# Kernel optimization log

Measured on AMD Instinct MI355X. Metric: run time of the kernel, lower is better.

## Reference

```python
import jax, jax.numpy as jnp
import numpy as np
from jax import lax

B, CH, TS = 64, 9, 3000
D, H, EMB = 64, 256, 32
WIDTHS = (3, 2, 2, 2, 2, 2)
IN_CH = (1, H, H, H, H, H)
OUT_CH = (H, H, H, H, H, D)


def setup_inputs():
    keys = iter(jax.random.split(jax.random.key(0), 64))
    inp = {"x": jax.random.normal(next(keys), (B, CH, TS), jnp.float32)}
    for l, (ci, co, w) in enumerate(zip(IN_CH, OUT_CH, WIDTHS)):
        inp[f"conv_w{l}"] = jax.random.normal(next(keys), (co, ci, w), jnp.float32) / np.float32(np.sqrt(ci * w))
        inp[f"conv_b{l}"] = jnp.zeros((co,), jnp.float32)
        inp[f"gn_g{l}"] = jnp.ones((co,), jnp.float32)
        inp[f"gn_b{l}"] = jnp.zeros((co,), jnp.float32)
    inp["ro_w"] = jax.random.normal(next(keys), (D, D), jnp.float32) / np.float32(np.sqrt(D))
    inp["ro_b"] = jnp.zeros((D,), jnp.float32)
    for r in range(2):
        inp[f"msg_w{r}"] = jax.random.normal(next(keys), (2 * D, D), jnp.float32) / np.float32(np.sqrt(2 * D))
        inp[f"msg_b{r}"] = jnp.zeros((D,), jnp.float32)
    inp["rn_w1"] = jax.random.normal(next(keys), (D, D), jnp.float32) / np.float32(np.sqrt(D))
    inp["rn_b1"] = jnp.zeros((D,), jnp.float32)
    inp["rn_w2"] = jax.random.normal(next(keys), (D, D), jnp.float32) / np.float32(np.sqrt(D))
    inp["rn_b2"] = jnp.zeros((D,), jnp.float32)
    inp["proj_w"] = jax.random.normal(next(keys), (D, EMB), jnp.float32) / np.float32(np.sqrt(D))
    inp["proj_b"] = jnp.zeros((EMB,), jnp.float32)
    return inp


def _gn(h, g, b):
    # GroupNorm(num_groups=1): normalize over (C, T) per sample
    mu = h.mean(axis=(1, 2), keepdims=True)
    var = h.var(axis=(1, 2), keepdims=True)
    return (h - mu) * lax.rsqrt(var + 1e-5) * g[None, :, None] + b[None, :, None]


def _forward(x, ps):
    b, ch, ts = x.shape
    h = x.reshape(b * ch, 1, ts)  # each view is one 1-channel node signal
    for l, w in enumerate(WIDTHS):
        W, bi, g, be = ps[4 * l], ps[4 * l + 1], ps[4 * l + 2], ps[4 * l + 3]
        h = lax.conv_general_dilated(h, W, (w,), [(w // 2, w // 2)], dimension_numbers=("NCH", "OIH", "NCH")) + bi[None, :, None]
        h = jax.nn.gelu(_gn(h, g, be), approximate=False)
    ro_w, ro_b = ps[24], ps[25]
    h = jnp.einsum("nct,co->not", h, ro_w) + ro_b[None, :, None]  # 1x1 readout conv
    lat = h.transpose(0, 2, 1)  # [b*ch, T, D]
    N = b * ch
    # fully-connected graph within each sample, exactly as in the torch code
    msg_from = np.repeat(np.arange(N), ch - 1)
    grid = np.broadcast_to(np.arange(N).reshape(b, ch)[:, None, :], (b, ch, ch))
    msg_to = grid[:, ~np.eye(ch, dtype=bool)].reshape(-1)
    for W, bi in ((ps[26], ps[27]), (ps[28], ps[29])):
        m = jnp.concatenate([lat[msg_from], lat[msg_to]], axis=-1)  # [E, T, 2D]
        m = jax.nn.relu(m @ W + bi) / (ch - 1)  # dropout is identity at eval
        lat = lat.at[msg_to].add(m)
    view_id = np.repeat(np.arange(b), ch)
    y = jax.ops.segment_sum(lat, view_id, num_segments=b)  # [b, T, D]
    y = (jax.nn.relu(y @ ps[30] + ps[31]) @ ps[32] + ps[33]) / ch
    return (y @ ps[34] + ps[35]).transpose(0, 2, 1)  # [b, EMB, T]


def reference(x, conv_w0, conv_b0, gn_g0, gn_b0, conv_w1, conv_b1, gn_g1, gn_b1, conv_w2, conv_b2, gn_g2, gn_b2, conv_w3, conv_b3, gn_g3, gn_b3, conv_w4, conv_b4, gn_g4, gn_b4, conv_w5, conv_b5, gn_g5, gn_b5, ro_w, ro_b, msg_w0, msg_b0, msg_w1, msg_b1, rn_w1, rn_b1, rn_w2, rn_b2, proj_w, proj_b):
    ps = (conv_w0, conv_b0, gn_g0, gn_b0, conv_w1, conv_b1, gn_g1, gn_b1, conv_w2, conv_b2, gn_g2, gn_b2, conv_w3, conv_b3, gn_g3, gn_b3, conv_w4, conv_b4, gn_g4, gn_b4, conv_w5, conv_b5, gn_g5, gn_b5, ro_w, ro_b, msg_w0, msg_b0, msg_w1, msg_b1, rn_w1, rn_b1, rn_w2, rn_b2, proj_w, proj_b)
    return _forward(x, ps)
```

## Files before the change

### kernel.cpp

```cpp
#include <hip/hip_runtime.h>
#include <hip/hip_bf16.h>

typedef __hip_bfloat16 bf16;
typedef __attribute__((ext_vector_type(8))) short s8v;
typedef __attribute__((ext_vector_type(4))) float f4v;

__device__ __forceinline__ float erf_approx(float x) {
    float ax = fabsf(x);
    float t = __builtin_amdgcn_rcpf(__builtin_fmaf(0.3275911f, ax, 1.0f));
    float p = t * (0.254829592f + t * (-0.284496736f + t * (1.421413741f
              + t * (-1.453152027f + t * 1.061405429f))));
    float r = 1.0f - p * __expf(-ax * ax);
    return copysignf(r, x);
}
__device__ __forceinline__ float gelu_f(float v) {
    return 0.5f * v * (1.f + erf_approx(v * 0.70710678118654752440f));
}
__device__ __forceinline__ unsigned short f2bf_u(float f) {
    bf16 b = __float2bfloat16(f);
    return *(unsigned short*)&b;
}
__device__ __forceinline__ float bfu2f(unsigned short u) {
    bf16 b = *(bf16*)&u;
    return __bfloat162float(b);
}

__global__ __launch_bounds__(256) void zero_k(float* __restrict__ p, int n) {
    int i = blockIdx.x * 256 + threadIdx.x;
    if (i < n) p[i] = 0.f;
}

__global__ __launch_bounds__(256) void wcvt_k(
    const float* __restrict__ w1, const float* __restrict__ w2,
    const float* __restrict__ w3, const float* __restrict__ w4,
    const float* __restrict__ w5, bf16* __restrict__ dst)
{
    int i = blockIdx.x * 256 + threadIdx.x;
    if (i >= 557056) return;
    const float* src; int li;
    if      (i < 131072) { src = w1; li = i; }
    else if (i < 262144) { src = w2; li = i - 131072; }
    else if (i < 393216) { src = w3; li = i - 262144; }
    else if (i < 524288) { src = w4; li = i - 393216; }
    else                 { src = w5; li = i - 524288; }
    int co = li >> 9, rem = li & 511;
    int kc = rem >> 6, rr = rem & 63;
    int s = rr >> 5, cil = rr & 31;
    dst[i] = __float2bfloat16(src[co * 512 + (kc * 32 + cil) * 2 + s]);
}

__global__ __launch_bounds__(256) void m0red_k(
    const float* __restrict__ W0, const float* __restrict__ b0, float* __restrict__ coef)
{
    __shared__ float red[256];
    const int co = threadIdx.x;
    float w0 = W0[3 * co], w1 = W0[3 * co + 1], w2 = W0[3 * co + 2], b = b0[co];
    float vals[14] = {w0, w1, w2, b,
                      w0 * w0, w1 * w1, w2 * w2, b * b,
                      2.f * w0 * w1, 2.f * w0 * w2, 2.f * w1 * w2,
                      2.f * w0 * b, 2.f * w1 * b, 2.f * w2 * b};
    for (int k = 0; k < 14; k++) {
        red[co] = vals[k];
        __syncthreads();
        for (int st = 128; st > 0; st >>= 1) {
            if (co < st) red[co] += red[co + st];
            __syncthreads();
        }
        if (co == 0) coef[k] = red[0];
        __syncthreads();
    }
}

__global__ __launch_bounds__(256) void c0stats_k(
    const float* __restrict__ x, const float* __restrict__ coef,
    float* __restrict__ mu0, float* __restrict__ rstd0)
{
    __shared__ float xsl[3008];
    __shared__ float red[512];
    const int n = blockIdx.x, tid = threadIdx.x;
    const float* xr = x + (size_t)n * 3000;
    for (int i = tid; i < 750; i += 256) *(float4*)&xsl[4 + 4 * i] = *(const float4*)(xr + 4 * i);
    if (tid < 4) xsl[tid] = 0.f;
    float c[14];
    #pragma unroll
    for (int k = 0; k < 14; k++) c[k] = coef[k];
    __syncthreads();
    float S = 0.f, Q = 0.f;
    if (tid < 250) {
        float f[16];
        #pragma unroll
        for (int k = 0; k < 4; k++) *(float4*)&f[4 * k] = *(const float4*)&xsl[12 * tid + 4 * k];
        #pragma unroll
        for (int j = 0; j < 4; j++) {
            float x0 = f[3 * j + 3], x1 = f[3 * j + 4], x2 = f[3 * j + 5];
            S += c[0] * x0 + c[1] * x1 + c[2] * x2 + c[3];
            Q += c[4] * x0 * x0 + c[5] * x1 * x1 + c[6] * x2 * x2 + c[7]
               + c[8] * x0 * x1 + c[9] * x0 * x2 + c[10] * x1 * x2
               + c[11] * x0 + c[12] * x1 + c[13] * x2;
        }
    }
    red[tid] = S; red[256 + tid] = Q;
    __syncthreads();
    for (int st = 128; st > 0; st >>= 1) {
        if (tid < st) { red[tid] += red[tid + st]; red[256 + tid] += red[256 + tid + st]; }
        __syncthreads();
    }
    if (tid == 0) {
        float m = red[0] * (1.f / 256000.f);
        float var = red[256] * (1.f / 256000.f) - m * m;
        mu0[n] = m;
        rstd0[n] = rsqrtf(var + 1e-5f);
    }
}

__global__ __launch_bounds__(256) void h0gT_k(
    const float* __restrict__ x, const float* __restrict__ W0,
    const float* __restrict__ b0, const float* __restrict__ g0,
    const float* __restrict__ be0, const float* __restrict__ mu0,
    const float* __restrict__ rstd0, bf16* __restrict__ h0gT, int n0)
{
    __shared__ float xs[96];
    __shared__ float w0s[768];
    __shared__ float aco[256], cco[256];
    const int z = blockIdx.y;
    const int n = n0 + z;
    const int t0 = blockIdx.x * 32;
    const int tid = threadIdx.x;
    for (int i = tid; i < 768; i += 256) w0s[i] = W0[i];
    {
        float mu = mu0[n], rs = rstd0[n];
        float a = rs * g0[tid];
        aco[tid] = a;
        cco[tid] = (b0[tid] - mu) * a + be0[tid];
    }
    if (tid < 96) {
        int xg = 3 * t0 - 1 + tid;
        xs[tid] = (xg >= 0 && xg < 3000) ? x[(size_t)n * 3000 + xg] : 0.f;
    }
    __syncthreads();
    const int oct = tid & 31, ci0 = oct * 8;
    const int tq = tid >> 5;
    #pragma unroll
    for (int u = 0; u < 4; u++) {
        int tl = tq + 8 * u;
        int t = t0 + tl;
        if (t >= 1000) continue;
        float x0 = xs[3 * tl], x1 = xs[3 * tl + 1], x2 = xs[3 * tl + 2];
        ushort4 lo, hi;
        unsigned short* pu = (unsigned short*)&lo;
        #pragma unroll
        for (int jj = 0; jj < 8; jj++) {
            int ci = ci0 + jj;
            float conv = w0s[3 * ci] * x0 + w0s[3 * ci + 1] * x1 + w0s[3 * ci + 2] * x2;
            float v = gelu_f(conv * aco[ci] + cco[ci]);
            if (jj < 4) pu[jj] = f2bf_u(v);
            else ((unsigned short*)&hi)[jj - 4] = f2bf_u(v);
        }
        bf16* orow = h0gT + ((size_t)z * 1000 + t) * 256 + ci0;
        *(ushort4*)orow = lo;
        *(ushort4*)(orow + 4) = hi;
    }
}

template<int MW, int NW, bool FUSE>
__global__ __launch_bounds__(256) void convT_k(
    const bf16* __restrict__ g, const bf16* __restrict__ Wp,
    const float* __restrict__ bias, bf16* __restrict__ hout,
    float* __restrict__ ssum, float* __restrict__ ssq,
    int T_g, int T_out, int n0,
    const float* __restrict__ pssum, const float* __restrict__ pssq,
    const float* __restrict__ pgam, const float* __restrict__ pbet,
    float pinvCT)
{
    constexpr int CO = 4 * NW * 16;
    constexpr int MT = MW * 16;
    constexpr int NSLOT = MT * 8;
    constexpr int NU = (NSLOT + 255) / 256;
    __shared__ bf16 aT[MT * 64];
    __shared__ float biasS[CO];
    __shared__ float red[512];
    __shared__ float acoS[256], ccoS[256];
    const int n  = blockIdx.y;
    const int t0 = blockIdx.x * MT;
    const int tid = threadIdx.x;
    for (int i = tid; i < CO; i += 256) biasS[i] = bias[i];
    if (FUSE) {
        float mu = pssum[n0 + n] * pinvCT;
        float rs = rsqrtf(pssq[n0 + n] * pinvCT - mu * mu + 1e-5f);
        float a = rs * pgam[tid];
        acoS[tid] = a;
        ccoS[tid] = pbet[tid] - mu * a;
        __syncthreads();
    }
    const int w = tid >> 6, lane = tid & 63;
    const int l16 = lane & 15, quad = lane >> 4;
    const int sx = l16 & 7;
    const bf16* gb = g + (size_t)n * T_g * 256;

    bool s_inv[NU];
    int s_q[NU], s_tin[NU], s_off[NU];
    #pragma unroll
    for (int u = 0; u < NU; u++) {
        int slot = tid + 256 * u;
        s_inv[u] = (NSLOT % 256 != 0) && (slot >= NSLOT);
        if (s_inv[u]) { s_tin[u] = 0x7fffffff; s_q[u] = 0; s_off[u] = 0; continue; }
        int t = slot >> 3, j = slot & 7;
        int ks = j >> 2, q = j & 3;
        s_q[u] = q;
        s_tin[u] = 2 * (t0 + t) - 1 + ks;
        s_off[u] = (t * 8 + (j ^ (t & 7))) * 8;
    }

    f4v acc[MW][NW];
    #pragma unroll
    for (int i = 0; i < MW; i++)
        #pragma unroll
        for (int j = 0; j < NW; j++) acc[i][j] = (f4v){0.f, 0.f, 0.f, 0.f};

    auto act8 = [&](s8v v, int ci0) -> s8v {
        if (FUSE) {
            float4 a0 = *(const float4*)&acoS[ci0], a1 = *(const float4*)&acoS[ci0 + 4];
            float4 c0 = *(const float4*)&ccoS[ci0], c1 = *(const float4*)&ccoS[ci0 + 4];
            float av[8] = {a0.x, a0.y, a0.z, a0.w, a1.x, a1.y, a1.z, a1.w};
            float cv[8] = {c0.x, c0.y, c0.z, c0.w, c1.x, c1.y, c1.z, c1.w};
            unsigned short* uu = (unsigned short*)&v;
            #pragma unroll
            for (int jj = 0; jj < 8; jj++)
                uu[jj] = f2bf_u(gelu_f(bfu2f(uu[jj]) * av[jj] + cv[jj]));
        }
        return v;
    };

    for (int kc = 0; kc < 8; kc++) {
        #pragma unroll
        for (int u = 0; u < NU; u++) {
            if (s_inv[u]) continue;
            int tin = s_tin[u];
            s8v v = (s8v){0, 0, 0, 0, 0, 0, 0, 0};
            if ((unsigned)tin < (unsigned)T_g)
                v = act8(*(const s8v*)(gb + (size_t)tin * 256 + kc * 32 + s_q[u] * 8),
                         kc * 32 + s_q[u] * 8);
            *(s8v*)&aT[s_off[u]] = v;
        }
        s8v bfr[2][NW];
        #pragma unroll
        for (int ks = 0; ks < 2; ks++)
            #pragma unroll
            for (int j = 0; j < NW; j++) {
                int co = w * NW * 16 + j * 16 + l16;
                bfr[ks][j] = *(const s8v*)(Wp + (size_t)co * 512 + kc * 64 + ks * 32 + quad * 8);
            }
        __syncthreads();
        #pragma unroll
        for (int ks = 0; ks < 2; ks++) {
            const int sl = (ks * 4 + quad) ^ sx;
            s8v af[MW];
            #pragma unroll
            for (int i = 0; i < MW; i++)
                af[i] = *(const s8v*)&aT[(i * 16 + l16) * 64 + sl * 8];
            #pragma unroll
            for (int i = 0; i < MW; i++)
                #pragma unroll
                for (int j = 0; j < NW; j++)
                    acc[i][j] = __builtin_amdgcn_mfma_f32_16x16x32_bf16(af[i], bfr[ks][j], acc[i][j], 0, 0, 0);
        }
        __syncthreads();
    }

    float lsum = 0.f, lsq = 0.f;
    #pragma unroll
    for (int i = 0; i < MW; i++) {
        #pragma unroll
        for (int r = 0; r < 4; r++) {
            int t = t0 + i * 16 + quad * 4 + r;
            if (t < T_out) {
                bf16* orow = hout + ((size_t)n * T_out + t) * CO;
                #pragma unroll
                for (int j = 0; j < NW; j++) {
                    int co = w * NW * 16 + j * 16 + l16;
                    float v = acc[i][j][r] + biasS[co];
                    orow[co] = __float2bfloat16(v);
                    lsum += v; lsq += v * v;
                }
            }
        }
    }
    red[tid] = lsum; red[256 + tid] = lsq;
    __syncthreads();
    for (int st = 128; st > 0; st >>= 1) {
        if (tid < st) { red[tid] += red[tid + st]; red[256 + tid] += red[256 + tid + st]; }
        __syncthreads();
    }
    if (tid == 0) { atomicAdd(&ssum[n0 + n], red[0]); atomicAdd(&ssq[n0 + n], red[256]); }
}

__global__ __launch_bounds__(256) void readout_pre_k(
    const bf16* __restrict__ h5T, const float* __restrict__ row,
    const float* __restrict__ rob, const float* __restrict__ g5,
    const float* __restrict__ be5, const float* __restrict__ ssum,
    const float* __restrict__ ssq, float invCT,
    const float* __restrict__ mw, const float* __restrict__ mb,
    float* __restrict__ lat0, float* __restrict__ A0, float* __restrict__ Bv0)
{
    __shared__ float lh[2112];
    __shared__ float ll[2112];
    __shared__ float lw[8192];
    __shared__ float lb[64];
    const int n = blockIdx.x, tid = threadIdx.x;
    const float mu = ssum[n] * invCT;
    const float rs = rsqrtf(ssq[n] * invCT - mu * mu + 1e-5f);
    for (int idx = tid; idx < 2112; idx += 256) {
        int c = idx & 63;
        float a = rs * g5[c];
        float v = __bfloat162float(h5T[(size_t)n * 2112 + idx]) * a + (be5[c] - mu * a);
        lh[idx] = gelu_f(v);
    }
    for (int idx = tid; idx < 4096; idx += 256) lw[idx] = row[idx];
    if (tid < 64) lb[tid] = rob[tid];
    __syncthreads();
    for (int idx = tid; idx < 2112; idx += 256) {
        int t = idx >> 6, d = idx & 63;
        float a = lb[d];
        #pragma unroll 8
        for (int c = 0; c < 64; c++) a += lh[t * 64 + c] * lw[c * 64 + d];
        ll[idx] = a;
        lat0[(size_t)n * 2112 + idx] = a;
    }
    __syncthreads();
    for (int idx = tid; idx < 8192; idx += 256) lw[idx] = mw[idx];
    if (tid < 64) lb[tid] = mb[tid];
    __syncthreads();
    for (int idx = tid; idx < 2112; idx += 256) {
        int t = idx >> 6, d = idx & 63;
        float a = 0.f, bb = lb[d];
        #pragma unroll 8
        for (int k = 0; k < 64; k++) {
            float xv = ll[t * 64 + k];
            a  += xv * lw[k * 64 + d];
            bb += xv * lw[(64 + k) * 64 + d];
        }
        A0[(size_t)n * 2112 + idx]  = a;
        Bv0[(size_t)n * 2112 + idx] = bb;
    }
}

__global__ __launch_bounds__(256) void comb_pre_k(
    const float* __restrict__ lat0, const float* __restrict__ A0,
    const float* __restrict__ Bv0, const float* __restrict__ mw,
    const float* __restrict__ mb, float* __restrict__ lat1,
    float* __restrict__ A1, float* __restrict__ Bv1)
{
    __shared__ float ll[2112];
    __shared__ float lw[8192];
    __shared__ float lb[64];
    const int n = blockIdx.x, tid = threadIdx.x;
    const int b9 = (n / 9) * 9, j = n - b9;
    for (int idx = tid; idx < 2112; idx += 256) {
        float base = Bv0[(size_t)n * 2112 + idx];
        float s = 0.f;
        #pragma unroll
        for (int i = 0; i < 9; i++) {
            if (i == j) continue;
            s += fmaxf(A0[(size_t)(b9 + i) * 2112 + idx] + base, 0.f);
        }
        float v = lat0[(size_t)n * 2112 + idx] + s * 0.125f;
        ll[idx] = v;
        lat1[(size_t)n * 2112 + idx] = v;
    }
    for (int idx = tid; idx < 8192; idx += 256) lw[idx] = mw[idx];
    if (tid < 64) lb[tid] = mb[tid];
    __syncthreads();
    for (int idx = tid; idx < 2112; idx += 256) {
        int t = idx >> 6, d = idx & 63;
        float a = 0.f, bb = lb[d];
        #pragma unroll 8
        for (int k = 0; k < 64; k++) {
            float xv = ll[t * 64 + k];
            a  += xv * lw[k * 64 + d];
            bb += xv * lw[(64 + k) * 64 + d];
        }
        A1[(size_t)n * 2112 + idx]  = a;
        Bv1[(size_t)n * 2112 + idx] = bb;
    }
}

__global__ __launch_bounds__(256) void final2_k(
    const float* __restrict__ lat1, const float* __restrict__ A1,
    const float* __restrict__ Bv1,
    const float* __restrict__ w1, const float* __restrict__ b1,
    const float* __restrict__ w2, const float* __restrict__ b2,
    const float* __restrict__ pw, const float* __restrict__ pb,
    float* __restrict__ out)
{
    __shared__ float ly[2112], lz[2112];
    __shared__ float lw1[4096], lw2[4096], lpw[2048];
    __shared__ float lb1[64], lb2[64], lpb[32];
    const int b = blockIdx.x, tid = threadIdx.x;
    for (int idx = tid; idx < 4096; idx += 256) { lw1[idx] = w1[idx]; lw2[idx] = w2[idx]; }
    for (int idx = tid; idx < 2048; idx += 256) lpw[idx] = pw[idx];
    if (tid < 64) { lb1[tid] = b1[tid]; lb2[tid] = b2[tid]; }
    if (tid < 32) lpb[tid] = pb[tid];
    for (int idx = tid; idx < 2112; idx += 256) {
        float Av[9], Bb[9], s = 0.f;
        #pragma unroll
        for (int jj = 0; jj < 9; jj++) {
            size_t off = ((size_t)(b * 9 + jj)) * 2112 + idx;
            Av[jj] = A1[off];
            Bb[jj] = Bv1[off];
            s += lat1[off];
        }
        float m = 0.f;
        #pragma unroll
        for (int jj = 0; jj < 9; jj++) {
            float rowsum = 0.f;
            #pragma unroll
            for (int ii = 0; ii < 9; ii++) rowsum += fmaxf(Av[ii] + Bb[jj], 0.f);
            m += rowsum - fmaxf(Av[jj] + Bb[jj], 0.f);
        }
        ly[idx] = s + m * 0.125f;
    }
    __syncthreads();
    for (int idx = tid; idx < 2112; idx += 256) {
        int t = idx >> 6, d = idx & 63;
        float s = lb1[d];
        #pragma unroll 8
        for (int k = 0; k < 64; k++) s += ly[t * 64 + k] * lw1[k * 64 + d];
        lz[idx] = fmaxf(s, 0.f);
    }
    __syncthreads();
    for (int idx = tid; idx < 2112; idx += 256) {
        int t = idx >> 6, d = idx & 63;
        float s = lb2[d];
        #pragma unroll 8
        for (int k = 0; k < 64; k++) s += lz[t * 64 + k] * lw2[k * 64 + d];
        ly[idx] = s * (1.f / 9.f);
    }
    __syncthreads();
    for (int idx = tid; idx < 1056; idx += 256) {
        int e = idx / 33, t = idx - e * 33;
        float s = lpb[e];
        #pragma unroll 8
        for (int d = 0; d < 64; d++) s += ly[t * 64 + d] * lpw[d * 32 + e];
        out[(size_t)b * 1056 + idx] = s;
    }
}

extern "C" void kernel_launch(void* const* d_in, const int* in_sizes, int n_in,
                              void* d_out, int out_size, void* d_ws, size_t ws_size,
                              hipStream_t stream)
{
    const float* x = (const float*)d_in[0];
    const float* cw[6]; const float* cb[6]; const float* gg[6]; const float* gb[6];
    for (int l = 0; l < 6; l++) {
        cw[l] = (const float*)d_in[1 + 4 * l];
        cb[l] = (const float*)d_in[2 + 4 * l];
        gg[l] = (const float*)d_in[3 + 4 * l];
        gb[l] = (const float*)d_in[4 + 4 * l];
    }
    const float* ro_w = (const float*)d_in[25];
    const float* ro_b = (const float*)d_in[26];
    const float* mw0  = (const float*)d_in[27];
    const float* mb0  = (const float*)d_in[28];
    const float* mw1  = (const float*)d_in[29];
    const float* mb1  = (const float*)d_in[30];
    const float* rw1  = (const float*)d_in[31];
    const float* rb1  = (const float*)d_in[32];
    const float* rw2  = (const float*)d_in[33];
    const float* rb2  = (const float*)d_in[34];
    const float* pw   = (const float*)d_in[35];
    const float* pb   = (const float*)d_in[36];

    char* ws = (char*)d_ws;
    bf16* h1T  = (bf16*)(ws);
    bf16* h0gT = (bf16*)(ws + 147750912);
    bf16* h2T  = (bf16*)(ws + 147750912);
    bf16* h3T  = (bf16*)(ws + 221773824);
    bf16* h4T  = (bf16*)(ws);
    bf16* h5T  = (bf16*)(ws + 147750912);
    float* lat0 = (float*)(ws);
    float* A0   = lat0 + 1216512;
    float* Bv0  = A0   + 1216512;
    float* lat1 = Bv0  + 1216512;
    float* A1   = lat1 + 1216512;
    float* Bv1  = A1   + 1216512;
    float* stat  = (float*)(ws + 258932736);
    float* mu0   = stat;
    float* rstd0 = stat + 576;
    float* coef  = stat + 1152;
    float* ssumA = stat + 1168;
    float* ssqA  = ssumA + 5 * 576;
    bf16*  Wp    = (bf16*)(ws + 258965504);
    #define SSUM(l) (ssumA + ((l) - 1) * 576)
    #define SSQ(l)  (ssqA  + ((l) - 1) * 576)

    zero_k<<<(5760 + 255) / 256, 256, 0, stream>>>(ssumA, 2 * 5 * 576);
    wcvt_k<<<(557056 + 255) / 256, 256, 0, stream>>>(cw[1], cw[2], cw[3], cw[4], cw[5], Wp);
    m0red_k<<<1, 256, 0, stream>>>(cw[0], cb[0], coef);
    c0stats_k<<<576, 256, 0, stream>>>(x, coef, mu0, rstd0);

    for (int c = 0; c < 3; c++) {
        int n0 = c * 192;
        h0gT_k<<<dim3(32, 192), 256, 0, stream>>>(x, cw[0], cb[0], gg[0], gb[0], mu0, rstd0, h0gT, n0);
        convT_k<4, 4, false><<<dim3(8, 192), 256, 0, stream>>>(
            h0gT, Wp, cb[1], h1T + (size_t)n0 * 501 * 256, SSUM(1), SSQ(1), 1000, 501, n0,
            nullptr, nullptr, nullptr, nullptr, 0.f);
    }

    convT_k<4, 4, true><<<dim3(4, 576), 256, 0, stream>>>(
        h1T, Wp + 131072, cb[2], h2T, SSUM(2), SSQ(2), 501, 251, 0,
        SSUM(1), SSQ(1), gg[1], gb[1], 1.f / (256.f * 501.f));

    convT_k<4, 4, true><<<dim3(2, 576), 256, 0, stream>>>(
        h2T, Wp + 262144, cb[3], h3T, SSUM(3), SSQ(3), 251, 126, 0,
        SSUM(2), SSQ(2), gg[2], gb[2], 1.f / (256.f * 251.f));

    convT_k<4, 4, true><<<dim3(1, 576), 256, 0, stream>>>(
        h3T, Wp + 393216, cb[4], h4T, SSUM(4), SSQ(4), 126, 64, 0,
        SSUM(3), SSQ(3), gg[3], gb[3], 1.f / (256.f * 126.f));

    convT_k<3, 1, true><<<dim3(1, 576), 256, 0, stream>>>(
        h4T, Wp + 524288, cb[5], h5T, SSUM(5), SSQ(5), 64, 33, 0,
        SSUM(4), SSQ(4), gg[4], gb[4], 1.f / (256.f * 64.f));

    readout_pre_k<<<576, 256, 0, stream>>>(h5T, ro_w, ro_b, gg[5], gb[5],
                                           SSUM(5), SSQ(5), 1.f / (64.f * 33.f),
                                           mw0, mb0, lat0, A0, Bv0);
    comb_pre_k<<<576, 256, 0, stream>>>(lat0, A0, Bv0, mw1, mb1, lat1, A1, Bv1);
    final2_k<<<64, 256, 0, stream>>>(lat1, A1, Bv1, rw1, rb1, rw2, rb2, pw, pb, (float*)d_out);
}
```

Baseline: 769.0 us.

## Fuse layer-0 conv+GroupNorm+GELU into the layer-1 MFMA conv kernel

Removes the separate h0gT kernel that wrote the full layer-0 activation (576x1000x256 bf16) to memory. The layer-1 conv now loads raw input samples and transposed layer-0 taps into shared memory and computes conv, norm and GELU on the fly while staging its A tile. This also drops the three-chunk launch loop in favour of a single launch. In exchange each tile recomputes layer-0 values with extra ALU and erf work per element, and a redundant duplicate load remains in the MODE 1 path.

```diff
diff --git a/kernel.cpp b/kernel.cpp
--- a/kernel.cpp
+++ b/kernel.cpp
@@ -50,11 +50,13 @@
 }
 
 __global__ __launch_bounds__(256) void m0red_k(
-    const float* __restrict__ W0, const float* __restrict__ b0, float* __restrict__ coef)
+    const float* __restrict__ W0, const float* __restrict__ b0,
+    float* __restrict__ coef, float* __restrict__ w0t)
 {
     __shared__ float red[256];
     const int co = threadIdx.x;
     float w0 = W0[3 * co], w1 = W0[3 * co + 1], w2 = W0[3 * co + 2], b = b0[co];
+    w0t[co] = w0; w0t[256 + co] = w1; w0t[512 + co] = w2;
     float vals[14] = {w0, w1, w2, b,
                       w0 * w0, w1 * w1, w2 * w2, b * b,
                       2.f * w0 * w1, 2.f * w0 * w2, 2.f * w1 * w2,
@@ -113,60 +115,12 @@
     }
 }
 
-__global__ __launch_bounds__(256) void h0gT_k(
-    const float* __restrict__ x, const float* __restrict__ W0,
-    const float* __restrict__ b0, const float* __restrict__ g0,
-    const float* __restrict__ be0, const float* __restrict__ mu0,
-    const float* __restrict__ rstd0, bf16* __restrict__ h0gT, int n0)
-{
-    __shared__ float xs[96];
-    __shared__ float w0s[768];
-    __shared__ float aco[256], cco[256];
-    const int z = blockIdx.y;
-    const int n = n0 + z;
-    const int t0 = blockIdx.x * 32;
-    const int tid = threadIdx.x;
-    for (int i = tid; i < 768; i += 256) w0s[i] = W0[i];
-    {
-        float mu = mu0[n], rs = rstd0[n];
-        float a = rs * g0[tid];
-        aco[tid] = a;
-        cco[tid] = (b0[tid] - mu) * a + be0[tid];
-    }
-    if (tid < 96) {
-        int xg = 3 * t0 - 1 + tid;
-        xs[tid] = (xg >= 0 && xg < 3000) ? x[(size_t)n * 3000 + xg] : 0.f;
-    }
-    __syncthreads();
-    const int oct = tid & 31, ci0 = oct * 8;
-    const int tq = tid >> 5;
-    #pragma unroll
-    for (int u = 0; u < 4; u++) {
-        int tl = tq + 8 * u;
-        int t = t0 + tl;
-        if (t >= 1000) continue;
-        float x0 = xs[3 * tl], x1 = xs[3 * tl + 1], x2 = xs[3 * tl + 2];
-        ushort4 lo, hi;
-        unsigned short* pu = (unsigned short*)&lo;
-        #pragma unroll
-        for (int jj = 0; jj < 8; jj++) {
-            int ci = ci0 + jj;
-            float conv = w0s[3 * ci] * x0 + w0s[3 * ci + 1] * x1 + w0s[3 * ci + 2] * x2;
-            float v = gelu_f(conv * aco[ci] + cco[ci]);
-            if (jj < 4) pu[jj] = f2bf_u(v);
-            else ((unsigned short*)&hi)[jj - 4] = f2bf_u(v);
-        }
-        bf16* orow = h0gT + ((size_t)z * 1000 + t) * 256 + ci0;
-        *(ushort4*)orow = lo;
-        *(ushort4*)(orow + 4) = hi;
-    }
-}
-
-template<int MW, int NW, bool FUSE>
+template<int MW, int NW, int MODE>
 __global__ __launch_bounds__(256) void convT_k(
-    const bf16* __restrict__ g, const bf16* __restrict__ Wp,
-    const float* __restrict__ bias, bf16* __restrict__ hout,
-    float* __restrict__ ssum, float* __restrict__ ssq,
+    const bf16* __restrict__ g, const float* __restrict__ xraw,
+    const float* __restrict__ w0t, const bf16* __restrict__ Wp,
+    const float* __restrict__ bias, const float* __restrict__ b0c,
+    bf16* __restrict__ hout, float* __restrict__ ssum, float* __restrict__ ssq,
     int T_g, int T_out, int n0,
     const float* __restrict__ pssum, const float* __restrict__ pssq,
     const float* __restrict__ pgam, const float* __restrict__ pbet,
@@ -180,22 +134,37 @@
     __shared__ float biasS[CO];
     __shared__ float red[512];
     __shared__ float acoS[256], ccoS[256];
+    __shared__ float xs[(MODE == 2) ? 400 : 1];
+    __shared__ float w0s[(MODE == 2) ? 768 : 1];
     const int n  = blockIdx.y;
     const int t0 = blockIdx.x * MT;
     const int tid = threadIdx.x;
     for (int i = tid; i < CO; i += 256) biasS[i] = bias[i];
-    if (FUSE) {
+    if (MODE == 1) {
         float mu = pssum[n0 + n] * pinvCT;
         float rs = rsqrtf(pssq[n0 + n] * pinvCT - mu * mu + 1e-5f);
         float a = rs * pgam[tid];
         acoS[tid] = a;
         ccoS[tid] = pbet[tid] - mu * a;
         __syncthreads();
+    } else {
+        float mu = pssum[n];
+        float rs = pssq[n];
+        float a = rs * pgam[tid];
+        acoS[tid] = a;
+        ccoS[tid] = (b0c[tid] - mu) * a + pbet[tid];
+        for (int i = tid; i < 768; i += 256) w0s[i] = w0t[i];
+        const float* xr = xraw + (size_t)n * 3000;
+        for (int i = tid; i < 400; i += 256) {
+            int xg = 6 * t0 - 4 + i;
+            xs[i] = ((unsigned)xg < 3000u) ? xr[xg] : 0.f;
+        }
+        __syncthreads();
     }
     const int w = tid >> 6, lane = tid & 63;
     const int l16 = lane & 15, quad = lane >> 4;
     const int sx = l16 & 7;
-    const bf16* gb = g + (size_t)n * T_g * 256;
+    const bf16* gb = (MODE == 2) ? nullptr : (g + (size_t)n * T_g * 256);
 
     bool s_inv[NU];
     int s_q[NU], s_tin[NU], s_off[NU];
@@ -217,29 +186,41 @@
         #pragma unroll
         for (int j = 0; j < NW; j++) acc[i][j] = (f4v){0.f, 0.f, 0.f, 0.f};
 
-    auto act8 = [&](s8v v, int ci0) -> s8v {
-        if (FUSE) {
-            float4 a0 = *(const float4*)&acoS[ci0], a1 = *(const float4*)&acoS[ci0 + 4];
-            float4 c0 = *(const float4*)&ccoS[ci0], c1 = *(const float4*)&ccoS[ci0 + 4];
-            float av[8] = {a0.x, a0.y, a0.z, a0.w, a1.x, a1.y, a1.z, a1.w};
-            float cv[8] = {c0.x, c0.y, c0.z, c0.w, c1.x, c1.y, c1.z, c1.w};
-            unsigned short* uu = (unsigned short*)&v;
-            #pragma unroll
-            for (int jj = 0; jj < 8; jj++)
-                uu[jj] = f2bf_u(gelu_f(bfu2f(uu[jj]) * av[jj] + cv[jj]));
-        }
-        return v;
-    };
-
     for (int kc = 0; kc < 8; kc++) {
         #pragma unroll
         for (int u = 0; u < NU; u++) {
             if (s_inv[u]) continue;
             int tin = s_tin[u];
             s8v v = (s8v){0, 0, 0, 0, 0, 0, 0, 0};
-            if ((unsigned)tin < (unsigned)T_g)
-                v = act8(*(const s8v*)(gb + (size_t)tin * 256 + kc * 32 + s_q[u] * 8),
-                         kc * 32 + s_q[u] * 8);
+            if ((unsigned)tin < (unsigned)T_g) {
+                const int ci0 = kc * 32 + s_q[u] * 8;
+                float4 a0 = *(const float4*)&acoS[ci0], a1 = *(const float4*)&acoS[ci0 + 4];
+                float4 c0 = *(const float4*)&ccoS[ci0], c1 = *(const float4*)&ccoS[ci0 + 4];
+                float av[8] = {a0.x, a0.y, a0.z, a0.w, a1.x, a1.y, a1.z, a1.w};
+                float cv[8] = {c0.x, c0.y, c0.z, c0.w, c1.x, c1.y, c1.z, c1.w};
+                unsigned short* uu = (unsigned short*)&v;
+                if (MODE == 2) {
+                    int lx = 3 * (tin - 2 * t0) + 3;
+                    float x0 = xs[lx], x1 = xs[lx + 1], x2 = xs[lx + 2];
+                    float4 wa0 = *(const float4*)&w0s[ci0],       wa1 = *(const float4*)&w0s[ci0 + 4];
+                    float4 wb0 = *(const float4*)&w0s[256 + ci0], wb1 = *(const float4*)&w0s[256 + ci0 + 4];
+                    float4 wc0 = *(const float4*)&w0s[512 + ci0], wc1 = *(const float4*)&w0s[512 + ci0 + 4];
+                    float wav[8] = {wa0.x, wa0.y, wa0.z, wa0.w, wa1.x, wa1.y, wa1.z, wa1.w};
+                    float wbv[8] = {wb0.x, wb0.y, wb0.z, wb0.w, wb1.x, wb1.y, wb1.z, wb1.w};
+                    float wcv[8] = {wc0.x, wc0.y, wc0.z, wc0.w, wc1.x, wc1.y, wc1.z, wc1.w};
+                    #pragma unroll
+                    for (int jj = 0; jj < 8; jj++) {
+                        float conv = wav[jj] * x0 + wbv[jj] * x1 + wcv[jj] * x2;
+                        uu[jj] = f2bf_u(gelu_f(conv * av[jj] + cv[jj]));
+                    }
+                } else {
+                    v = *(const s8v*)(gb + (size_t)tin * 256 + ci0 - kc * 32 + kc * 32 + s_q[u] * 8 - s_q[u] * 8);
+                    v = *(const s8v*)(gb + (size_t)tin * 256 + kc * 32 + s_q[u] * 8);
+                    #pragma unroll
+                    for (int jj = 0; jj < 8; jj++)
+                        uu[jj] = f2bf_u(gelu_f(bfu2f(uu[jj]) * av[jj] + cv[jj]));
+                }
+            }
             *(s8v*)&aT[s_off[u]] = v;
         }
         s8v bfr[2][NW];
@@ -472,7 +453,6 @@
 
     char* ws = (char*)d_ws;
     bf16* h1T  = (bf16*)(ws);
-    bf16* h0gT = (bf16*)(ws + 147750912);
     bf16* h2T  = (bf16*)(ws + 147750912);
     bf16* h3T  = (bf16*)(ws + 221773824);
     bf16* h4T  = (bf16*)(ws);
@@ -489,37 +469,34 @@
     float* coef  = stat + 1152;
     float* ssumA = stat + 1168;
     float* ssqA  = ssumA + 5 * 576;
+    float* w0taps = ssqA + 5 * 576;
     bf16*  Wp    = (bf16*)(ws + 258965504);
     #define SSUM(l) (ssumA + ((l) - 1) * 576)
     #define SSQ(l)  (ssqA  + ((l) - 1) * 576)
 
     zero_k<<<(5760 + 255) / 256, 256, 0, stream>>>(ssumA, 2 * 5 * 576);
     wcvt_k<<<(557056 + 255) / 256, 256, 0, stream>>>(cw[1], cw[2], cw[3], cw[4], cw[5], Wp);
-    m0red_k<<<1, 256, 0, stream>>>(cw[0], cb[0], coef);
+    m0red_k<<<1, 256, 0, stream>>>(cw[0], cb[0], coef, w0taps);
     c0stats_k<<<576, 256, 0, stream>>>(x, coef, mu0, rstd0);
 
-    for (int c = 0; c < 3; c++) {
-        int n0 = c * 192;
-        h0gT_k<<<dim3(32, 192), 256, 0, stream>>>(x, cw[0], cb[0], gg[0], gb[0], mu0, rstd0, h0gT, n0);
-        convT_k<4, 4, false><<<dim3(8, 192), 256, 0, stream>>>(
-            h0gT, Wp, cb[1], h1T + (size_t)n0 * 501 * 256, SSUM(1), SSQ(1), 1000, 501, n0,
-            nullptr, nullptr, nullptr, nullptr, 0.f);
-    }
-
-    convT_k<4, 4, true><<<dim3(4, 576), 256, 0, stream>>>(
-        h1T, Wp + 131072, cb[2], h2T, SSUM(2), SSQ(2), 501, 251, 0,
+    convT_k<4, 4, 2><<<dim3(8, 576), 256, 0, stream>>>(
+        nullptr, x, w0taps, Wp, cb[1], cb[0], h1T, SSUM(1), SSQ(1), 1000, 501, 0,
+        mu0, rstd0, gg[0], gb[0], 0.f);
+
+    convT_k<4, 4, 1><<<dim3(4, 576), 256, 0, stream>>>(
+        h1T, nullptr, nullptr, Wp + 131072, cb[2], nullptr, h2T, SSUM(2), SSQ(2), 501, 251, 0,
         SSUM(1), SSQ(1), gg[1], gb[1], 1.f / (256.f * 501.f));
 
-    convT_k<4, 4, true><<<dim3(2, 576), 256, 0, stream>>>(
-        h2T, Wp + 262144, cb[3], h3T, SSUM(3), SSQ(3), 251, 126, 0,
+    convT_k<4, 4, 1><<<dim3(2, 576), 256, 0, stream>>>(
+        h2T, nullptr, nullptr, Wp + 262144, cb[3], nullptr, h3T, SSUM(3), SSQ(3), 251, 126, 0,
         SSUM(2), SSQ(2), gg[2], gb[2], 1.f / (256.f * 251.f));
 
-    convT_k<4, 4, true><<<dim3(1, 576), 256, 0, stream>>>(
-        h3T, Wp + 393216, cb[4], h4T, SSUM(4), SSQ(4), 126, 64, 0,
+    convT_k<4, 4, 1><<<dim3(1, 576), 256, 0, stream>>>(
+        h3T, nullptr, nullptr, Wp + 393216, cb[4], nullptr, h4T, SSUM(4), SSQ(4), 126, 64, 0,
         SSUM(3), SSQ(3), gg[3], gb[3], 1.f / (256.f * 126.f));
 
-    convT_k<3, 1, true><<<dim3(1, 576), 256, 0, stream>>>(
-        h4T, Wp + 524288, cb[5], h5T, SSUM(5), SSQ(5), 64, 33, 0,
+    convT_k<3, 1, 1><<<dim3(1, 576), 256, 0, stream>>>(
+        h4T, nullptr, nullptr, Wp + 524288, cb[5], nullptr, h5T, SSUM(5), SSQ(5), 64, 33, 0,
         SSUM(4), SSQ(4), gg[4], gb[4], 1.f / (256.f * 64.f));
 
     readout_pre_k<<<576, 256, 0, stream>>>(h5T, ro_w, ro_b, gg[5], gb[5],
```

Result: faster. 673.9 us (-12.4%).
